# Performance work log

Measured on AMD Instinct MI355X. Metric: run time of the kernel, lower is better.

## Reference

```python
import jax, jax.numpy as jnp
import numpy as np

B, H, W, C, A, K = 1_000_000, 4, 4, 3, 4, 20
# slicing offsets (w_offset, h_offset) exactly as in the torch code
OFFSETS = [(0, 1), (2, 1), (1, 0), (1, 2)]


def setup_inputs() -> dict:
    key = jax.random.key(0)
    k0, k1, k2, k3, k4, k5 = jax.random.split(key, 6)
    obs = jax.random.normal(k0, (B, H, W, C), dtype=jnp.float32)
    # channel 1 encodes the agent position: exactly one nonzero per sample
    pos = jax.random.randint(k1, (B,), 0, H * W)
    ch1 = jnp.zeros((B, H * W), jnp.float32).at[jnp.arange(B), pos].set(1.0)
    obs = obs.at[..., 1].set(ch1.reshape(B, H, W)).reshape(B, H * W * C)
    s = 0.05  # keep |p| < 1 mostly so the K-step VI recursion stays bounded
    return {
        'obs': obs,
        'Phi_W': jax.random.normal(k2, (48, 48), jnp.float32) * s,
        'Phi_b': jax.random.normal(k3, (48,), jnp.float32) * s,
        'Logit_W': jax.random.normal(k4, (A, 36), jnp.float32) * s,
        'Logit_b': jax.random.normal(k5, (A,), jnp.float32) * s,
    }


def _pad2(x):
    # zero-pad last two spatial dims of (B, H, W) by 1
    return jnp.pad(x, ((0, 0), (1, 1), (1, 1)))


def reference(obs, Phi_W, Phi_b, Logit_W, Logit_b):
    out = (obs @ Phi_W.T + Phi_b).reshape(B, H, W, C)
    rin, rout, p = out[..., 0], out[..., 1], out[..., 2]
    rin_pad = _pad2(rin)  # (B, 6, 6)

    def step(v, _):
        vp = _pad2(v)  # (B, 6, 6)
        for wo, ho in OFFSETS:
            nv = p * vp[:, ho:ho + H, wo:wo + W] + rin_pad[:, ho:ho + H, wo:wo + W] - rout
            v = jnp.maximum(v, nv)
        return v, None

    V, _ = jax.lax.scan(step, jnp.zeros((B, H, W), jnp.float32), None, length=K)

    # agent position: first nonzero of channel 1 (row-major), default (1,1) -> flat 5
    obs4 = obs.reshape(B, H, W, C)
    nz = (obs4[..., 1] != 0).reshape(B, H * W)
    idx = jnp.where(nz.any(axis=1), jnp.argmax(nz, axis=1), 5)
    i, j = idx // W, idx % W

    # 3x3 windows around (i, j) in zero-padded state / value maps
    obs_pad = jnp.pad(obs4, ((0, 0), (1, 1), (1, 1), (0, 0)))  # (B, 6, 6, 3)
    V_pad = _pad2(V)                                            # (B, 6, 6)
    d = jnp.arange(3)
    rows = i[:, None, None] + d[:, None]   # (B, 3, 1)
    cols = j[:, None, None] + d[None, :]   # (B, 1, 3)
    bb = jnp.arange(B)[:, None, None]
    sub_state = obs_pad[bb, rows, cols]    # (B, 3, 3, 3)
    sub_v = V_pad[bb, rows, cols]          # (B, 3, 3)

    logit_in = jnp.concatenate([sub_state.reshape(B, 27), sub_v.reshape(B, 9)], axis=1)
    logit = logit_in @ Logit_W.T + Logit_b  # (B, A)
    return logit
```

## Files before the change

### kernel.cpp

```cpp
#include <hip/hip_runtime.h>

#define BT 256
#define WREG 9216

#define MEMFENCE asm volatile("" ::: "memory")

typedef __attribute__((ext_vector_type(8))) short short8;
typedef __attribute__((ext_vector_type(4))) float f32x4;
typedef __attribute__((ext_vector_type(4))) unsigned int u32x4;
typedef _Float16 h2 __attribute__((ext_vector_type(2)));

__device__ inline unsigned cvtpkbf(float a, float b) {
    unsigned d;
    asm("v_cvt_pk_bf16_f32 %0, %1, %2" : "=v"(d) : "v"(a), "v"(b));
    return d;
}
__device__ inline float b2f(short s) {
    unsigned u = ((unsigned)(unsigned short)s) << 16;
    return __builtin_bit_cast(float, u);
}
__device__ inline unsigned pkrtz(float a, float b) {
    unsigned d;
    asm("v_cvt_pkrtz_f16_f32 %0, %1, %2" : "=v"(d) : "v"(a), "v"(b));
    return d;
}
__device__ inline unsigned pkfma(unsigned a, unsigned b, unsigned c) {
    unsigned d;
    asm("v_pk_fma_f16 %0, %1, %2, %3" : "=v"(d) : "v"(a), "v"(b), "v"(c));
    return d;
}
__device__ inline unsigned pkmax(unsigned a, unsigned b) {
    unsigned d;
    asm("v_pk_max_f16 %0, %1, %2" : "=v"(d) : "v"(a), "v"(b));
    return d;
}
__device__ inline unsigned pksub(unsigned a, unsigned b) {
    unsigned d;
    asm("v_pk_add_f16 %0, %1, %2 neg_lo:[0,1] neg_hi:[0,1]" : "=v"(d) : "v"(a), "v"(b));
    return d;
}
__device__ inline unsigned pkneg(unsigned b) {
    unsigned d;
    asm("v_pk_add_f16 %0, 0, %1 neg_lo:[0,1] neg_hi:[0,1]" : "=v"(d) : "v"(b));
    return d;
}

__device__ inline void vistep(const unsigned (&S)[4][2], unsigned (&D)[4][2],
                              const unsigned (&pp)[4][2],
                              const unsigned (&aL)[4][2], const unsigned (&aR)[4][2],
                              const unsigned (&aU)[4][2], const unsigned (&aD)[4][2])
{
    unsigned shl[4], shr[4];
    #pragma unroll
    for (int h = 0; h < 4; ++h) {
        shl[h] = S[h][1] << 16;
        shr[h] = S[h][0] >> 16;
    }
    #pragma unroll
    for (int h = 0; h < 4; ++h)
        #pragma unroll
        for (int j = 0; j < 2; ++j) {
            unsigned vL = j ? S[h][0] : shl[h];
            unsigned vR = j ? shr[h] : S[h][1];
            unsigned tU = (h > 0) ? pkfma(pp[h][j], S[h-1][j], aU[h][j]) : aU[h][j];
            unsigned tD = (h < 3) ? pkfma(pp[h][j], S[h+1][j], aD[h][j]) : aD[h][j];
            unsigned m1 = pkmax(S[h][j], pkfma(pp[h][j], vL, aL[h][j]));
            unsigned m2 = pkmax(pkfma(pp[h][j], vR, aR[h][j]), tU);
            D[h][j] = pkmax(pkmax(m1, m2), tD);
        }
}

__global__ __launch_bounds__(BT, 4) void vin_kernel(
    const float* __restrict__ obs,
    const float* __restrict__ PhiW,
    const float* __restrict__ Phib,
    const float* __restrict__ LW,
    const float* __restrict__ Lb,
    float* __restrict__ out, int Btot)
{
    __shared__ __align__(16) char smem[4 * WREG];
    const int tid  = threadIdx.x;
    const int lane = tid & 63;
    const int wid  = tid >> 6;
    const int b    = blockIdx.x * BT + tid;
    if (b >= Btot) return;

    char* wbase = smem + wid * WREG;
    const int jn = lane & 15;
    const int g  = lane >> 4;

    float o[48];
    {
        const float4* g4 = reinterpret_cast<const float4*>(obs + (size_t)b * 48);
        #pragma unroll
        for (int q = 0; q < 12; ++q) {
            float4 t = g4[q];
            o[4*q+0] = t.x; o[4*q+1] = t.y; o[4*q+2] = t.z; o[4*q+3] = t.w;
        }
    }

    float sidx = 0.0f;
    #pragma unroll
    for (int k = 1; k < 16; ++k)
        sidx = fmaf(o[k*3 + 1], (float)k, sidx);
    const int idx = (int)(sidx + 0.5f);
    const int ai = idx >> 2;
    const int aj = idx & 3;

    short8 bfrag[3][2];
    #pragma unroll
    for (int n = 0; n < 3; ++n) {
        const float* wrow = PhiW + (16*n + jn) * 48;
        float4 q0 = *reinterpret_cast<const float4*>(wrow + 8*g);
        float4 q1 = *reinterpret_cast<const float4*>(wrow + 8*g + 4);
        u32x4 t0;
        t0[0] = cvtpkbf(q0.x, q0.y); t0[1] = cvtpkbf(q0.z, q0.w);
        t0[2] = cvtpkbf(q1.x, q1.y); t0[3] = cvtpkbf(q1.z, q1.w);
        bfrag[n][0] = __builtin_bit_cast(short8, t0);
        u32x4 tz = {0u, 0u, 0u, 0u};
        if (g < 2) {
            float4 q2 = *reinterpret_cast<const float4*>(wrow + 32 + 8*g);
            float4 q3 = *reinterpret_cast<const float4*>(wrow + 36 + 8*g);
            tz[0] = cvtpkbf(q2.x, q2.y); tz[1] = cvtpkbf(q2.z, q2.w);
            tz[2] = cvtpkbf(q3.x, q3.y); tz[3] = cvtpkbf(q3.z, q3.w);
        }
        bfrag[n][1] = __builtin_bit_cast(short8, tz);
    }

    {
        u32x4* arow = reinterpret_cast<u32x4*>(wbase + lane * 144);
        #pragma unroll
        for (int q = 0; q < 6; ++q) {
            u32x4 v;
            #pragma unroll
            for (int e = 0; e < 4; ++e)
                v[e] = cvtpkbf(o[q*8 + 2*e], o[q*8 + 2*e + 1]);
            arow[q] = v;
        }
        u32x4 z = {0u, 0u, 0u, 0u};
        arow[6] = z; arow[7] = z;
    }
    MEMFENCE;

    float lg0 = Lb[0], lg1 = Lb[1], lg2 = Lb[2], lg3 = Lb[3];
    {
        const short* myobs = reinterpret_cast<const short*>(wbase + lane * 144);
        #pragma unroll
        for (int dh = 0; dh < 3; ++dh)
            #pragma unroll
            for (int dw = 0; dw < 3; ++dw) {
                int r = ai + dh - 1, c = aj + dw - 1;
                bool ok = ((unsigned)r < 4u) && ((unsigned)c < 4u);
                int ba = ok ? (r*4 + c) * 3 : 48;
                float s0 = b2f(myobs[ba+0]);
                float s1 = b2f(myobs[ba+1]);
                float s2 = b2f(myobs[ba+2]);
                int f = (dh*3 + dw) * 3;
                lg0 = fmaf(s0, LW[0*36+f], fmaf(s1, LW[0*36+f+1], fmaf(s2, LW[0*36+f+2], lg0)));
                lg1 = fmaf(s0, LW[1*36+f], fmaf(s1, LW[1*36+f+1], fmaf(s2, LW[1*36+f+2], lg1)));
                lg2 = fmaf(s0, LW[2*36+f], fmaf(s1, LW[2*36+f+1], fmaf(s2, LW[2*36+f+2], lg2)));
                lg3 = fmaf(s0, LW[3*36+f], fmaf(s1, LW[3*36+f+1], fmaf(s2, LW[3*36+f+2], lg3)));
            }
    }

    short8 afrag[4][2];
    #pragma unroll
    for (int m = 0; m < 4; ++m) {
        const char* rp = wbase + (m*16 + jn) * 144;
        afrag[m][0] = *reinterpret_cast<const short8*>(rp + 16*g);
        afrag[m][1] = *reinterpret_cast<const short8*>(rp + 64 + 16*g);
    }
    MEMFENCE;

    float rinf[16], routf[16], pcf[16];
    const float bias[3] = {Phib[jn], Phib[16 + jn], Phib[32 + jn]};
    #pragma unroll
    for (int n = 0; n < 3; ++n) {
        f32x4 acc[4];
        #pragma unroll
        for (int m = 0; m < 4; ++m) {
            float bn = bias[n];
            acc[m] = (f32x4){bn, bn, bn, bn};
            acc[m] = __builtin_amdgcn_mfma_f32_16x16x32_bf16(afrag[m][0], bfrag[n][0], acc[m], 0, 0, 0);
            acc[m] = __builtin_amdgcn_mfma_f32_16x16x32_bf16(afrag[m][1], bfrag[n][1], acc[m], 0, 0, 0);
        }
        #pragma unroll
        for (int m = 0; m < 4; ++m)
            #pragma unroll
            for (int r = 0; r < 4; ++r) {
                int row = m*16 + g*4 + r;
                reinterpret_cast<float*>(wbase + row * 144)[jn] = acc[m][r];
            }
        MEMFENCE;
        const char* myrow = wbase + lane * 144;
        #pragma unroll
        for (int q = 0; q < 4; ++q) {
            f32x4 t = *reinterpret_cast<const f32x4*>(myrow + q * 16);
            #pragma unroll
            for (int e = 0; e < 4; ++e) {
                int c = 16*n + 4*q + e;
                int cell = c / 3, ch = c - 3*cell;
                if (ch == 0)      rinf[cell]  = t[e];
                else if (ch == 1) routf[cell] = t[e];
                else              pcf[cell]   = t[e];
            }
        }
        MEMFENCE;
    }

    unsigned rinp[4][2], routp[4][2], pp[4][2];
    #pragma unroll
    for (int h = 0; h < 4; ++h)
        #pragma unroll
        for (int j = 0; j < 2; ++j) {
            int c0 = 4*h + j, c1 = 4*h + j + 2;
            rinp[h][j]  = pkrtz(rinf[c0], rinf[c1]);
            routp[h][j] = pkrtz(routf[c0], routf[c1]);
            pp[h][j]    = pkrtz(pcf[c0], pcf[c1]);
        }
    unsigned aL2[4][2], aR2[4][2], aU2[4][2], aD2[4][2];
    #pragma unroll
    for (int h = 0; h < 4; ++h) {
        aL2[h][0] = pksub(rinp[h][1] << 16, routp[h][0]);
        aL2[h][1] = pksub(rinp[h][0], routp[h][1]);
        aR2[h][0] = pksub(rinp[h][1], routp[h][0]);
        aR2[h][1] = pksub(rinp[h][0] >> 16, routp[h][1]);
        #pragma unroll
        for (int j = 0; j < 2; ++j) {
            aU2[h][j] = (h > 0) ? pksub(rinp[h-1][j], routp[h][j]) : pkneg(routp[0][j]);
            aD2[h][j] = (h < 3) ? pksub(rinp[h+1][j], routp[h][j]) : pkneg(routp[3][j]);
        }
    }

    unsigned Vp[4][2], Vn[4][2];
    #pragma unroll
    for (int h = 0; h < 4; ++h) { Vp[h][0] = 0u; Vp[h][1] = 0u; }
    #pragma unroll 1
    for (int s = 0; s < 10; ++s) {
        vistep(Vp, Vn, pp, aL2, aR2, aU2, aD2);
        vistep(Vn, Vp, pp, aL2, aR2, aU2, aD2);
    }

    {
        char* myrow = wbase + lane * 144;
        #pragma unroll
        for (int h = 0; h < 4; ++h) {
            h2 a = __builtin_bit_cast(h2, Vp[h][0]);
            h2 c = __builtin_bit_cast(h2, Vp[h][1]);
            *reinterpret_cast<f32x4*>(myrow + h * 16) =
                (f32x4){(float)a[0], (float)c[0], (float)a[1], (float)c[1]};
        }
        *reinterpret_cast<float*>(myrow + 64) = 0.0f;
    }
    MEMFENCE;
    {
        const float* myv = reinterpret_cast<const float*>(wbase + lane * 144);
        #pragma unroll
        for (int dh = 0; dh < 3; ++dh)
            #pragma unroll
            for (int dw = 0; dw < 3; ++dw) {
                int r = ai + dh - 1, c = aj + dw - 1;
                bool ok = ((unsigned)r < 4u) && ((unsigned)c < 4u);
                int ba = ok ? (r*4 + c) : 16;
                float v = myv[ba];
                int f = 27 + dh*3 + dw;
                lg0 = fmaf(v, LW[0*36+f], lg0);
                lg1 = fmaf(v, LW[1*36+f], lg1);
                lg2 = fmaf(v, LW[2*36+f], lg2);
                lg3 = fmaf(v, LW[3*36+f], lg3);
            }
    }

    reinterpret_cast<float4*>(out)[b] = make_float4(lg0, lg1, lg2, lg3);
}

extern "C" void kernel_launch(void* const* d_in, const int* in_sizes, int n_in,
                              void* d_out, int out_size, void* d_ws, size_t ws_size,
                              hipStream_t stream) {
    const float* obs  = (const float*)d_in[0];
    const float* PhiW = (const float*)d_in[1];
    const float* Phib = (const float*)d_in[2];
    const float* LW   = (const float*)d_in[3];
    const float* Lb   = (const float*)d_in[4];
    float* out = (float*)d_out;

    const int Btot = in_sizes[0] / 48;
    const int grid = (Btot + BT - 1) / BT;
    hipLaunchKernelGGL(vin_kernel, dim3(grid), dim3(BT), 0, stream,
                       obs, PhiW, Phib, LW, Lb, out, Btot);
}
```

Baseline: 68.34 us.

## Load MFMA A-fragments directly from global and shrink LDS staging to raise occupancy

Instead of loading each sample's 48 floats into registers and staging bf16 rows in LDS for the MFMA A operand, lanes now read their A-fragment slices straight from global memory (other samples' rows) and convert to bf16. The 3x3 state window is read from global fp32 rather than LDS bf16, and PhiW fragments are loaded per n-iteration to cut live registers. The per-wave LDS region shrinks from 144-byte rows to 68-byte rows and launch bounds go from 4 to 5 waves/SIMD. The cost is strided and repeated global reads (relying on cache) and scalar LDS accesses in place of vector ones.

```diff
diff --git a/kernel.cpp b/kernel.cpp
--- a/kernel.cpp
+++ b/kernel.cpp
@@ -1,7 +1,8 @@
 #include <hip/hip_runtime.h>
 
 #define BT 256
-#define WREG 9216
+#define RSTRIDE 68
+#define WLDS (64 * RSTRIDE)
 
 #define MEMFENCE asm volatile("" ::: "memory")
 
@@ -14,10 +15,6 @@
     unsigned d;
     asm("v_cvt_pk_bf16_f32 %0, %1, %2" : "=v"(d) : "v"(a), "v"(b));
     return d;
-}
-__device__ inline float b2f(short s) {
-    unsigned u = ((unsigned)(unsigned short)s) << 16;
-    return __builtin_bit_cast(float, u);
 }
 __device__ inline unsigned pkrtz(float a, float b) {
     unsigned d;
@@ -70,7 +67,7 @@
         }
 }
 
-__global__ __launch_bounds__(BT, 4) void vin_kernel(
+__global__ __launch_bounds__(BT, 5) void vin_kernel(
     const float* __restrict__ obs,
     const float* __restrict__ PhiW,
     const float* __restrict__ Phib,
@@ -78,132 +75,113 @@
     const float* __restrict__ Lb,
     float* __restrict__ out, int Btot)
 {
-    __shared__ __align__(16) char smem[4 * WREG];
+    __shared__ __align__(16) char smem[4 * WLDS];
     const int tid  = threadIdx.x;
     const int lane = tid & 63;
     const int wid  = tid >> 6;
     const int b    = blockIdx.x * BT + tid;
     if (b >= Btot) return;
 
-    char* wbase = smem + wid * WREG;
+    char* wbase = smem + wid * WLDS;
     const int jn = lane & 15;
     const int g  = lane >> 4;
-
-    float o[48];
-    {
-        const float4* g4 = reinterpret_cast<const float4*>(obs + (size_t)b * 48);
-        #pragma unroll
-        for (int q = 0; q < 12; ++q) {
-            float4 t = g4[q];
-            o[4*q+0] = t.x; o[4*q+1] = t.y; o[4*q+2] = t.z; o[4*q+3] = t.w;
-        }
+    const float* myobs = obs + (size_t)b * 48;
+    const size_t wbsamp = (size_t)(blockIdx.x * BT + wid * 64);
+
+    short8 afrag[4][2];
+    #pragma unroll
+    for (int m = 0; m < 4; ++m) {
+        const float* sr = obs + (wbsamp + m*16 + jn) * 48;
+        float4 q0 = *reinterpret_cast<const float4*>(sr + 8*g);
+        float4 q1 = *reinterpret_cast<const float4*>(sr + 8*g + 4);
+        u32x4 t0;
+        t0[0] = cvtpkbf(q0.x, q0.y); t0[1] = cvtpkbf(q0.z, q0.w);
+        t0[2] = cvtpkbf(q1.x, q1.y); t0[3] = cvtpkbf(q1.z, q1.w);
+        afrag[m][0] = __builtin_bit_cast(short8, t0);
+        u32x4 tz = {0u, 0u, 0u, 0u};
+        if (g < 2) {
+            float4 q2 = *reinterpret_cast<const float4*>(sr + 32 + 8*g);
+            float4 q3 = *reinterpret_cast<const float4*>(sr + 36 + 8*g);
+            tz[0] = cvtpkbf(q2.x, q2.y); tz[1] = cvtpkbf(q2.z, q2.w);
+            tz[2] = cvtpkbf(q3.x, q3.y); tz[3] = cvtpkbf(q3.z, q3.w);
+        }
+        afrag[m][1] = __builtin_bit_cast(short8, tz);
     }
 
     float sidx = 0.0f;
     #pragma unroll
     for (int k = 1; k < 16; ++k)
-        sidx = fmaf(o[k*3 + 1], (float)k, sidx);
+        sidx = fmaf(myobs[3*k + 1], (float)k, sidx);
     const int idx = (int)(sidx + 0.5f);
     const int ai = idx >> 2;
     const int aj = idx & 3;
 
-    short8 bfrag[3][2];
-    #pragma unroll
-    for (int n = 0; n < 3; ++n) {
-        const float* wrow = PhiW + (16*n + jn) * 48;
-        float4 q0 = *reinterpret_cast<const float4*>(wrow + 8*g);
-        float4 q1 = *reinterpret_cast<const float4*>(wrow + 8*g + 4);
-        u32x4 t0;
-        t0[0] = cvtpkbf(q0.x, q0.y); t0[1] = cvtpkbf(q0.z, q0.w);
-        t0[2] = cvtpkbf(q1.x, q1.y); t0[3] = cvtpkbf(q1.z, q1.w);
-        bfrag[n][0] = __builtin_bit_cast(short8, t0);
-        u32x4 tz = {0u, 0u, 0u, 0u};
-        if (g < 2) {
-            float4 q2 = *reinterpret_cast<const float4*>(wrow + 32 + 8*g);
-            float4 q3 = *reinterpret_cast<const float4*>(wrow + 36 + 8*g);
-            tz[0] = cvtpkbf(q2.x, q2.y); tz[1] = cvtpkbf(q2.z, q2.w);
-            tz[2] = cvtpkbf(q3.x, q3.y); tz[3] = cvtpkbf(q3.z, q3.w);
-        }
-        bfrag[n][1] = __builtin_bit_cast(short8, tz);
-    }
-
-    {
-        u32x4* arow = reinterpret_cast<u32x4*>(wbase + lane * 144);
-        #pragma unroll
-        for (int q = 0; q < 6; ++q) {
-            u32x4 v;
-            #pragma unroll
-            for (int e = 0; e < 4; ++e)
-                v[e] = cvtpkbf(o[q*8 + 2*e], o[q*8 + 2*e + 1]);
-            arow[q] = v;
-        }
-        u32x4 z = {0u, 0u, 0u, 0u};
-        arow[6] = z; arow[7] = z;
-    }
-    MEMFENCE;
-
     float lg0 = Lb[0], lg1 = Lb[1], lg2 = Lb[2], lg3 = Lb[3];
-    {
-        const short* myobs = reinterpret_cast<const short*>(wbase + lane * 144);
-        #pragma unroll
-        for (int dh = 0; dh < 3; ++dh)
-            #pragma unroll
-            for (int dw = 0; dw < 3; ++dw) {
-                int r = ai + dh - 1, c = aj + dw - 1;
-                bool ok = ((unsigned)r < 4u) && ((unsigned)c < 4u);
-                int ba = ok ? (r*4 + c) * 3 : 48;
-                float s0 = b2f(myobs[ba+0]);
-                float s1 = b2f(myobs[ba+1]);
-                float s2 = b2f(myobs[ba+2]);
-                int f = (dh*3 + dw) * 3;
-                lg0 = fmaf(s0, LW[0*36+f], fmaf(s1, LW[0*36+f+1], fmaf(s2, LW[0*36+f+2], lg0)));
-                lg1 = fmaf(s0, LW[1*36+f], fmaf(s1, LW[1*36+f+1], fmaf(s2, LW[1*36+f+2], lg1)));
-                lg2 = fmaf(s0, LW[2*36+f], fmaf(s1, LW[2*36+f+1], fmaf(s2, LW[2*36+f+2], lg2)));
-                lg3 = fmaf(s0, LW[3*36+f], fmaf(s1, LW[3*36+f+1], fmaf(s2, LW[3*36+f+2], lg3)));
-            }
-    }
-
-    short8 afrag[4][2];
-    #pragma unroll
-    for (int m = 0; m < 4; ++m) {
-        const char* rp = wbase + (m*16 + jn) * 144;
-        afrag[m][0] = *reinterpret_cast<const short8*>(rp + 16*g);
-        afrag[m][1] = *reinterpret_cast<const short8*>(rp + 64 + 16*g);
-    }
-    MEMFENCE;
+    #pragma unroll
+    for (int dh = 0; dh < 3; ++dh)
+        #pragma unroll
+        for (int dw = 0; dw < 3; ++dw) {
+            int r = ai + dh - 1, c = aj + dw - 1;
+            bool ok = ((unsigned)r < 4u) && ((unsigned)c < 4u);
+            int ba = ok ? (r*4 + c) * 3 : 0;
+            float s0 = myobs[ba+0];
+            float s1 = myobs[ba+1];
+            float s2 = myobs[ba+2];
+            if (!ok) { s0 = 0.f; s1 = 0.f; s2 = 0.f; }
+            int f = (dh*3 + dw) * 3;
+            lg0 = fmaf(s0, LW[0*36+f], fmaf(s1, LW[0*36+f+1], fmaf(s2, LW[0*36+f+2], lg0)));
+            lg1 = fmaf(s0, LW[1*36+f], fmaf(s1, LW[1*36+f+1], fmaf(s2, LW[1*36+f+2], lg1)));
+            lg2 = fmaf(s0, LW[2*36+f], fmaf(s1, LW[2*36+f+1], fmaf(s2, LW[2*36+f+2], lg2)));
+            lg3 = fmaf(s0, LW[3*36+f], fmaf(s1, LW[3*36+f+1], fmaf(s2, LW[3*36+f+2], lg3)));
+        }
 
     float rinf[16], routf[16], pcf[16];
     const float bias[3] = {Phib[jn], Phib[16 + jn], Phib[32 + jn]};
     #pragma unroll
     for (int n = 0; n < 3; ++n) {
+        short8 bf0, bf1;
+        {
+            const float* wrow = PhiW + (16*n + jn) * 48;
+            float4 q0 = *reinterpret_cast<const float4*>(wrow + 8*g);
+            float4 q1 = *reinterpret_cast<const float4*>(wrow + 8*g + 4);
+            u32x4 t0;
+            t0[0] = cvtpkbf(q0.x, q0.y); t0[1] = cvtpkbf(q0.z, q0.w);
+            t0[2] = cvtpkbf(q1.x, q1.y); t0[3] = cvtpkbf(q1.z, q1.w);
+            bf0 = __builtin_bit_cast(short8, t0);
+            u32x4 tz = {0u, 0u, 0u, 0u};
+            if (g < 2) {
+                float4 q2 = *reinterpret_cast<const float4*>(wrow + 32 + 8*g);
+                float4 q3 = *reinterpret_cast<const float4*>(wrow + 36 + 8*g);
+                tz[0] = cvtpkbf(q2.x, q2.y); tz[1] = cvtpkbf(q2.z, q2.w);
+                tz[2] = cvtpkbf(q3.x, q3.y); tz[3] = cvtpkbf(q3.z, q3.w);
+            }
+            bf1 = __builtin_bit_cast(short8, tz);
+        }
         f32x4 acc[4];
         #pragma unroll
         for (int m = 0; m < 4; ++m) {
             float bn = bias[n];
             acc[m] = (f32x4){bn, bn, bn, bn};
-            acc[m] = __builtin_amdgcn_mfma_f32_16x16x32_bf16(afrag[m][0], bfrag[n][0], acc[m], 0, 0, 0);
-            acc[m] = __builtin_amdgcn_mfma_f32_16x16x32_bf16(afrag[m][1], bfrag[n][1], acc[m], 0, 0, 0);
+            acc[m] = __builtin_amdgcn_mfma_f32_16x16x32_bf16(afrag[m][0], bf0, acc[m], 0, 0, 0);
+            acc[m] = __builtin_amdgcn_mfma_f32_16x16x32_bf16(afrag[m][1], bf1, acc[m], 0, 0, 0);
         }
         #pragma unroll
         for (int m = 0; m < 4; ++m)
             #pragma unroll
             for (int r = 0; r < 4; ++r) {
                 int row = m*16 + g*4 + r;
-                reinterpret_cast<float*>(wbase + row * 144)[jn] = acc[m][r];
+                *reinterpret_cast<float*>(wbase + row * RSTRIDE + jn * 4) = acc[m][r];
             }
         MEMFENCE;
-        const char* myrow = wbase + lane * 144;
-        #pragma unroll
-        for (int q = 0; q < 4; ++q) {
-            f32x4 t = *reinterpret_cast<const f32x4*>(myrow + q * 16);
-            #pragma unroll
-            for (int e = 0; e < 4; ++e) {
-                int c = 16*n + 4*q + e;
-                int cell = c / 3, ch = c - 3*cell;
-                if (ch == 0)      rinf[cell]  = t[e];
-                else if (ch == 1) routf[cell] = t[e];
-                else              pcf[cell]   = t[e];
-            }
+        const char* myrow = wbase + lane * RSTRIDE;
+        #pragma unroll
+        for (int i = 0; i < 16; ++i) {
+            float t = *reinterpret_cast<const float*>(myrow + i * 4);
+            int c = 16*n + i;
+            int cell = c / 3, ch = c - 3*cell;
+            if (ch == 0)      rinf[cell]  = t;
+            else if (ch == 1) routf[cell] = t;
+            else              pcf[cell]   = t;
         }
         MEMFENCE;
     }
@@ -242,19 +220,21 @@
     }
 
     {
-        char* myrow = wbase + lane * 144;
+        char* myrow = wbase + lane * RSTRIDE;
         #pragma unroll
         for (int h = 0; h < 4; ++h) {
             h2 a = __builtin_bit_cast(h2, Vp[h][0]);
             h2 c = __builtin_bit_cast(h2, Vp[h][1]);
-            *reinterpret_cast<f32x4*>(myrow + h * 16) =
-                (f32x4){(float)a[0], (float)c[0], (float)a[1], (float)c[1]};
-        }
-        *reinterpret_cast<float*>(myrow + 64) = 0.0f;
+            reinterpret_cast<float*>(myrow)[4*h+0] = (float)a[0];
+            reinterpret_cast<float*>(myrow)[4*h+1] = (float)c[0];
+            reinterpret_cast<float*>(myrow)[4*h+2] = (float)a[1];
+            reinterpret_cast<float*>(myrow)[4*h+3] = (float)c[1];
+        }
+        reinterpret_cast<float*>(myrow)[16] = 0.0f;
     }
     MEMFENCE;
     {
-        const float* myv = reinterpret_cast<const float*>(wbase + lane * 144);
+        const float* myv = reinterpret_cast<const float*>(wbase + lane * RSTRIDE);
         #pragma unroll
         for (int dh = 0; dh < 3; ++dh)
             #pragma unroll
```

Result: slower. 126.4 us (+85.0%).

## Swizzle LDS rows, shrink scratch, and load Phi fragments per pass to cut registers

Applied to the files above, without the earlier changes.

Shrinks the per-wave LDS row stride from 144 to 128 bytes and applies an XOR swizzle so row accesses avoid bank conflicts despite the power-of-two stride. Phi weight fragments are now loaded per tile pass instead of all held up front. Observations are packed to bf16 while loading, and the projected outputs are unpacked straight into packed f16 registers instead of 48 float temporaries. Launch bounds rise to 5 blocks per SM to raise occupancy, at the risk of register spills and reloading weights three times.

```diff
diff --git a/kernel.cpp b/kernel.cpp
--- a/kernel.cpp
+++ b/kernel.cpp
@@ -1,7 +1,8 @@
 #include <hip/hip_runtime.h>
 
 #define BT 256
-#define WREG 9216
+#define ROWB 128
+#define WLDS (64 * ROWB)
 
 #define MEMFENCE asm volatile("" ::: "memory")
 
@@ -70,7 +71,55 @@
         }
 }
 
-__global__ __launch_bounds__(BT, 4) void vin_kernel(
+__device__ inline void tile_pass(int n, char* wbase, int jn, int g, int xb,
+                                 const short8 (&afrag)[4][2],
+                                 const float* __restrict__ PhiW, float bn,
+                                 float (&rv)[16])
+{
+    short8 bf0, bf1;
+    {
+        const float* wrow = PhiW + (16*n + jn) * 48;
+        float4 q0 = *reinterpret_cast<const float4*>(wrow + 8*g);
+        float4 q1 = *reinterpret_cast<const float4*>(wrow + 8*g + 4);
+        u32x4 t0;
+        t0[0] = cvtpkbf(q0.x, q0.y); t0[1] = cvtpkbf(q0.z, q0.w);
+        t0[2] = cvtpkbf(q1.x, q1.y); t0[3] = cvtpkbf(q1.z, q1.w);
+        bf0 = __builtin_bit_cast(short8, t0);
+        u32x4 tz = {0u, 0u, 0u, 0u};
+        if (g < 2) {
+            float4 q2 = *reinterpret_cast<const float4*>(wrow + 32 + 8*g);
+            float4 q3 = *reinterpret_cast<const float4*>(wrow + 36 + 8*g);
+            tz[0] = cvtpkbf(q2.x, q2.y); tz[1] = cvtpkbf(q2.z, q2.w);
+            tz[2] = cvtpkbf(q3.x, q3.y); tz[3] = cvtpkbf(q3.z, q3.w);
+        }
+        bf1 = __builtin_bit_cast(short8, tz);
+    }
+    f32x4 acc[4];
+    #pragma unroll
+    for (int m = 0; m < 4; ++m) {
+        acc[m] = (f32x4){bn, bn, bn, bn};
+        acc[m] = __builtin_amdgcn_mfma_f32_16x16x32_bf16(afrag[m][0], bf0, acc[m], 0, 0, 0);
+        acc[m] = __builtin_amdgcn_mfma_f32_16x16x32_bf16(afrag[m][1], bf1, acc[m], 0, 0, 0);
+    }
+    #pragma unroll
+    for (int m = 0; m < 4; ++m)
+        #pragma unroll
+        for (int r = 0; r < 4; ++r) {
+            int R = m*16 + 4*g + r;
+            int byte = R * ROWB + ((jn * 4) ^ (((4*g + r) & 7) << 4));
+            *reinterpret_cast<float*>(wbase + byte) = acc[m][r];
+        }
+    MEMFENCE;
+    char* myrow = wbase + ((threadIdx.x & 63) * ROWB);
+    #pragma unroll
+    for (int s = 0; s < 4; ++s) {
+        f32x4 t = *reinterpret_cast<const f32x4*>(myrow + ((s * 16) ^ xb));
+        rv[4*s+0] = t[0]; rv[4*s+1] = t[1]; rv[4*s+2] = t[2]; rv[4*s+3] = t[3];
+    }
+    MEMFENCE;
+}
+
+__global__ __launch_bounds__(BT, 5) void vin_kernel(
     const float* __restrict__ obs,
     const float* __restrict__ PhiW,
     const float* __restrict__ Phib,
@@ -78,146 +127,106 @@
     const float* __restrict__ Lb,
     float* __restrict__ out, int Btot)
 {
-    __shared__ __align__(16) char smem[4 * WREG];
+    __shared__ __align__(16) char smem[4 * WLDS];
     const int tid  = threadIdx.x;
     const int lane = tid & 63;
     const int wid  = tid >> 6;
     const int b    = blockIdx.x * BT + tid;
     if (b >= Btot) return;
 
-    char* wbase = smem + wid * WREG;
+    char* wbase = smem + wid * WLDS;
+    char* myrow = wbase + lane * ROWB;
     const int jn = lane & 15;
     const int g  = lane >> 4;
-
-    float o[48];
+    const int xb = (lane & 7) << 4;
+
+    unsigned op[24];
+    float sidx = 0.0f;
     {
         const float4* g4 = reinterpret_cast<const float4*>(obs + (size_t)b * 48);
         #pragma unroll
         for (int q = 0; q < 12; ++q) {
             float4 t = g4[q];
-            o[4*q+0] = t.x; o[4*q+1] = t.y; o[4*q+2] = t.z; o[4*q+3] = t.w;
-        }
-    }
-
-    float sidx = 0.0f;
-    #pragma unroll
-    for (int k = 1; k < 16; ++k)
-        sidx = fmaf(o[k*3 + 1], (float)k, sidx);
+            float va[4] = {t.x, t.y, t.z, t.w};
+            #pragma unroll
+            for (int e = 0; e < 4; ++e) {
+                int E = 4*q + e;
+                if ((E % 3) == 1 && (E / 3) > 0)
+                    sidx = fmaf(va[e], (float)(E / 3), sidx);
+            }
+            op[2*q]   = cvtpkbf(va[0], va[1]);
+            op[2*q+1] = cvtpkbf(va[2], va[3]);
+        }
+    }
     const int idx = (int)(sidx + 0.5f);
     const int ai = idx >> 2;
     const int aj = idx & 3;
 
-    short8 bfrag[3][2];
-    #pragma unroll
-    for (int n = 0; n < 3; ++n) {
-        const float* wrow = PhiW + (16*n + jn) * 48;
-        float4 q0 = *reinterpret_cast<const float4*>(wrow + 8*g);
-        float4 q1 = *reinterpret_cast<const float4*>(wrow + 8*g + 4);
-        u32x4 t0;
-        t0[0] = cvtpkbf(q0.x, q0.y); t0[1] = cvtpkbf(q0.z, q0.w);
-        t0[2] = cvtpkbf(q1.x, q1.y); t0[3] = cvtpkbf(q1.z, q1.w);
-        bfrag[n][0] = __builtin_bit_cast(short8, t0);
-        u32x4 tz = {0u, 0u, 0u, 0u};
-        if (g < 2) {
-            float4 q2 = *reinterpret_cast<const float4*>(wrow + 32 + 8*g);
-            float4 q3 = *reinterpret_cast<const float4*>(wrow + 36 + 8*g);
-            tz[0] = cvtpkbf(q2.x, q2.y); tz[1] = cvtpkbf(q2.z, q2.w);
-            tz[2] = cvtpkbf(q3.x, q3.y); tz[3] = cvtpkbf(q3.z, q3.w);
-        }
-        bfrag[n][1] = __builtin_bit_cast(short8, tz);
-    }
-
-    {
-        u32x4* arow = reinterpret_cast<u32x4*>(wbase + lane * 144);
+    {
         #pragma unroll
         for (int q = 0; q < 6; ++q) {
-            u32x4 v;
-            #pragma unroll
-            for (int e = 0; e < 4; ++e)
-                v[e] = cvtpkbf(o[q*8 + 2*e], o[q*8 + 2*e + 1]);
-            arow[q] = v;
+            u32x4 v = { op[4*q], op[4*q+1], op[4*q+2], op[4*q+3] };
+            *reinterpret_cast<u32x4*>(myrow + ((q * 16) ^ xb)) = v;
         }
         u32x4 z = {0u, 0u, 0u, 0u};
-        arow[6] = z; arow[7] = z;
+        *reinterpret_cast<u32x4*>(myrow + ((6 * 16) ^ xb)) = z;
+        *reinterpret_cast<u32x4*>(myrow + ((7 * 16) ^ xb)) = z;
     }
     MEMFENCE;
 
     float lg0 = Lb[0], lg1 = Lb[1], lg2 = Lb[2], lg3 = Lb[3];
-    {
-        const short* myobs = reinterpret_cast<const short*>(wbase + lane * 144);
-        #pragma unroll
-        for (int dh = 0; dh < 3; ++dh)
-            #pragma unroll
-            for (int dw = 0; dw < 3; ++dw) {
-                int r = ai + dh - 1, c = aj + dw - 1;
-                bool ok = ((unsigned)r < 4u) && ((unsigned)c < 4u);
-                int ba = ok ? (r*4 + c) * 3 : 48;
-                float s0 = b2f(myobs[ba+0]);
-                float s1 = b2f(myobs[ba+1]);
-                float s2 = b2f(myobs[ba+2]);
-                int f = (dh*3 + dw) * 3;
-                lg0 = fmaf(s0, LW[0*36+f], fmaf(s1, LW[0*36+f+1], fmaf(s2, LW[0*36+f+2], lg0)));
-                lg1 = fmaf(s0, LW[1*36+f], fmaf(s1, LW[1*36+f+1], fmaf(s2, LW[1*36+f+2], lg1)));
-                lg2 = fmaf(s0, LW[2*36+f], fmaf(s1, LW[2*36+f+1], fmaf(s2, LW[2*36+f+2], lg2)));
-                lg3 = fmaf(s0, LW[3*36+f], fmaf(s1, LW[3*36+f+1], fmaf(s2, LW[3*36+f+2], lg3)));
-            }
-    }
+    #pragma unroll
+    for (int dh = 0; dh < 3; ++dh)
+        #pragma unroll
+        for (int dw = 0; dw < 3; ++dw) {
+            int r = ai + dh - 1, c = aj + dw - 1;
+            bool ok = ((unsigned)r < 4u) && ((unsigned)c < 4u);
+            int ba = ok ? (r*4 + c) * 3 : 48;
+            float s0 = b2f(*reinterpret_cast<const short*>(myrow + (((ba+0)*2) ^ xb)));
+            float s1 = b2f(*reinterpret_cast<const short*>(myrow + (((ba+1)*2) ^ xb)));
+            float s2 = b2f(*reinterpret_cast<const short*>(myrow + (((ba+2)*2) ^ xb)));
+            int f = (dh*3 + dw) * 3;
+            lg0 = fmaf(s0, LW[0*36+f], fmaf(s1, LW[0*36+f+1], fmaf(s2, LW[0*36+f+2], lg0)));
+            lg1 = fmaf(s0, LW[1*36+f], fmaf(s1, LW[1*36+f+1], fmaf(s2, LW[1*36+f+2], lg1)));
+            lg2 = fmaf(s0, LW[2*36+f], fmaf(s1, LW[2*36+f+1], fmaf(s2, LW[2*36+f+2], lg2)));
+            lg3 = fmaf(s0, LW[3*36+f], fmaf(s1, LW[3*36+f+1], fmaf(s2, LW[3*36+f+2], lg3)));
+        }
 
     short8 afrag[4][2];
     #pragma unroll
     for (int m = 0; m < 4; ++m) {
-        const char* rp = wbase + (m*16 + jn) * 144;
-        afrag[m][0] = *reinterpret_cast<const short8*>(rp + 16*g);
-        afrag[m][1] = *reinterpret_cast<const short8*>(rp + 64 + 16*g);
-    }
-    MEMFENCE;
-
-    float rinf[16], routf[16], pcf[16];
-    const float bias[3] = {Phib[jn], Phib[16 + jn], Phib[32 + jn]};
-    #pragma unroll
-    for (int n = 0; n < 3; ++n) {
-        f32x4 acc[4];
-        #pragma unroll
-        for (int m = 0; m < 4; ++m) {
-            float bn = bias[n];
-            acc[m] = (f32x4){bn, bn, bn, bn};
-            acc[m] = __builtin_amdgcn_mfma_f32_16x16x32_bf16(afrag[m][0], bfrag[n][0], acc[m], 0, 0, 0);
-            acc[m] = __builtin_amdgcn_mfma_f32_16x16x32_bf16(afrag[m][1], bfrag[n][1], acc[m], 0, 0, 0);
-        }
-        #pragma unroll
-        for (int m = 0; m < 4; ++m)
-            #pragma unroll
-            for (int r = 0; r < 4; ++r) {
-                int row = m*16 + g*4 + r;
-                reinterpret_cast<float*>(wbase + row * 144)[jn] = acc[m][r];
-            }
-        MEMFENCE;
-        const char* myrow = wbase + lane * 144;
-        #pragma unroll
-        for (int q = 0; q < 4; ++q) {
-            f32x4 t = *reinterpret_cast<const f32x4*>(myrow + q * 16);
-            #pragma unroll
-            for (int e = 0; e < 4; ++e) {
-                int c = 16*n + 4*q + e;
-                int cell = c / 3, ch = c - 3*cell;
-                if (ch == 0)      rinf[cell]  = t[e];
-                else if (ch == 1) routf[cell] = t[e];
-                else              pcf[cell]   = t[e];
-            }
-        }
-        MEMFENCE;
-    }
+        const char* rp = wbase + (m*16 + jn) * ROWB;
+        const int xr = (jn & 7) << 4;
+        afrag[m][0] = *reinterpret_cast<const short8*>(rp + ((16*g) ^ xr));
+        afrag[m][1] = *reinterpret_cast<const short8*>(rp + ((64 + 16*g) ^ xr));
+    }
+    MEMFENCE;
 
     unsigned rinp[4][2], routp[4][2], pp[4][2];
-    #pragma unroll
-    for (int h = 0; h < 4; ++h)
-        #pragma unroll
-        for (int j = 0; j < 2; ++j) {
-            int c0 = 4*h + j, c1 = 4*h + j + 2;
-            rinp[h][j]  = pkrtz(rinf[c0], rinf[c1]);
-            routp[h][j] = pkrtz(routf[c0], routf[c1]);
-            pp[h][j]    = pkrtz(pcf[c0], pcf[c1]);
-        }
+    float rv[16];
+    const float b0 = Phib[jn], b1 = Phib[16 + jn], b2 = Phib[32 + jn];
+
+    tile_pass(0, wbase, jn, g, xb, afrag, PhiW, b0, rv);
+    rinp[0][0] = pkrtz(rv[0], rv[6]);  routp[0][0] = pkrtz(rv[1], rv[7]);  pp[0][0] = pkrtz(rv[2], rv[8]);
+    rinp[0][1] = pkrtz(rv[3], rv[9]);  routp[0][1] = pkrtz(rv[4], rv[10]); pp[0][1] = pkrtz(rv[5], rv[11]);
+    float c4r = rv[12], c4o = rv[13], c4p = rv[14], c5r = rv[15];
+
+    tile_pass(1, wbase, jn, g, xb, afrag, PhiW, b1, rv);
+    {
+        float c5o = rv[0], c5p = rv[1];
+        rinp[1][0] = pkrtz(c4r, rv[2]); routp[1][0] = pkrtz(c4o, rv[3]); pp[1][0] = pkrtz(c4p, rv[4]);
+        rinp[1][1] = pkrtz(c5r, rv[5]); routp[1][1] = pkrtz(c5o, rv[6]); pp[1][1] = pkrtz(c5p, rv[7]);
+    }
+    float c8r = rv[8],  c8o = rv[9],  c8p = rv[10];
+    float c9r = rv[11], c9o = rv[12], c9p = rv[13];
+    float c10r = rv[14], c10o = rv[15];
+
+    tile_pass(2, wbase, jn, g, xb, afrag, PhiW, b2, rv);
+    rinp[2][0] = pkrtz(c8r, c10r);     routp[2][0] = pkrtz(c8o, c10o);    pp[2][0] = pkrtz(c8p, rv[0]);
+    rinp[2][1] = pkrtz(c9r, rv[1]);    routp[2][1] = pkrtz(c9o, rv[2]);   pp[2][1] = pkrtz(c9p, rv[3]);
+    rinp[3][0] = pkrtz(rv[4], rv[10]); routp[3][0] = pkrtz(rv[5], rv[11]); pp[3][0] = pkrtz(rv[6], rv[12]);
+    rinp[3][1] = pkrtz(rv[7], rv[13]); routp[3][1] = pkrtz(rv[8], rv[14]); pp[3][1] = pkrtz(rv[9], rv[15]);
+
     unsigned aL2[4][2], aR2[4][2], aU2[4][2], aD2[4][2];
     #pragma unroll
     for (int h = 0; h < 4; ++h) {
@@ -242,34 +251,30 @@
     }
 
     {
-        char* myrow = wbase + lane * 144;
         #pragma unroll
         for (int h = 0; h < 4; ++h) {
             h2 a = __builtin_bit_cast(h2, Vp[h][0]);
             h2 c = __builtin_bit_cast(h2, Vp[h][1]);
-            *reinterpret_cast<f32x4*>(myrow + h * 16) =
+            *reinterpret_cast<f32x4*>(myrow + ((h * 16) ^ xb)) =
                 (f32x4){(float)a[0], (float)c[0], (float)a[1], (float)c[1]};
         }
-        *reinterpret_cast<float*>(myrow + 64) = 0.0f;
-    }
-    MEMFENCE;
-    {
-        const float* myv = reinterpret_cast<const float*>(wbase + lane * 144);
-        #pragma unroll
-        for (int dh = 0; dh < 3; ++dh)
-            #pragma unroll
-            for (int dw = 0; dw < 3; ++dw) {
-                int r = ai + dh - 1, c = aj + dw - 1;
-                bool ok = ((unsigned)r < 4u) && ((unsigned)c < 4u);
-                int ba = ok ? (r*4 + c) : 16;
-                float v = myv[ba];
-                int f = 27 + dh*3 + dw;
-                lg0 = fmaf(v, LW[0*36+f], lg0);
-                lg1 = fmaf(v, LW[1*36+f], lg1);
-                lg2 = fmaf(v, LW[2*36+f], lg2);
-                lg3 = fmaf(v, LW[3*36+f], lg3);
-            }
-    }
+        *reinterpret_cast<float*>(myrow + (64 ^ xb)) = 0.0f;
+    }
+    MEMFENCE;
+    #pragma unroll
+    for (int dh = 0; dh < 3; ++dh)
+        #pragma unroll
+        for (int dw = 0; dw < 3; ++dw) {
+            int r = ai + dh - 1, c = aj + dw - 1;
+            bool ok = ((unsigned)r < 4u) && ((unsigned)c < 4u);
+            int ba = ok ? (r*4 + c) : 16;
+            float v = *reinterpret_cast<const float*>(myrow + ((ba * 4) ^ xb));
+            int f = 27 + dh*3 + dw;
+            lg0 = fmaf(v, LW[0*36+f], lg0);
+            lg1 = fmaf(v, LW[1*36+f], lg1);
+            lg2 = fmaf(v, LW[2*36+f], lg2);
+            lg3 = fmaf(v, LW[3*36+f], lg3);
+        }
 
     reinterpret_cast<float4*>(out)[b] = make_float4(lg0, lg1, lg2, lg3);
 }
```

Measured after the change: 113.3 us. 65.8% more time.
